# Optimization experiments

Measured on AMD Instinct MI355X. Metric: run time of the kernel, lower is better.

Reference implementation:

```python
import jax, jax.numpy as jnp
import numpy as np

B, T, V, LMAX = 32, 1024, 1024, 128
BLANK = 0
NEG = jnp.float32(-1e30)


def setup_inputs() -> dict:
    key = jax.random.key(0)
    k1, k2, k3, k4 = jax.random.split(key, 4)
    ys_hat = jax.random.normal(k1, (B, T, V), dtype=jnp.float32)
    ys_pad = jax.random.randint(k2, (B, LMAX), 1, V, dtype=jnp.int32)  # no blanks in labels
    hlens = jax.random.randint(k3, (B,), T // 2, T + 1, dtype=jnp.int32)
    ys_lens = jax.random.randint(k4, (B,), LMAX // 2, LMAX + 1, dtype=jnp.int32)
    return {"ys_hat": ys_hat, "ys_pad": ys_pad, "hlens": hlens, "ys_lens": ys_lens}


def _ctc_neg_log_lik(log_probs, ys_pad, hlens, ys_lens):
    # log_probs: [B, T, V] log-softmaxed frame activations
    b, t, v = log_probs.shape
    lmax = ys_pad.shape[1]
    s = 2 * lmax + 1  # extended label length (blanks interleaved)
    # extended labels: blank, y1, blank, y2, ..., blank
    ext = jnp.full((b, s), BLANK, dtype=ys_pad.dtype).at[:, 1::2].set(ys_pad)  # [B, S]
    # gather per-frame log-probs of extended labels -> [B, T, S]
    lp_ext = jnp.take_along_axis(log_probs, jnp.broadcast_to(ext[:, None, :], (b, t, s)), axis=2)
    # skip transition allowed at s if ext[s] != blank and ext[s] != ext[s-2]
    ext_m2 = jnp.pad(ext[:, :-2], ((0, 0), (2, 0)), constant_values=BLANK)
    skip = (jnp.arange(s)[None, :] >= 2) & (ext != BLANK) & (ext != ext_m2)  # [B, S]

    def shift(a, n):
        return jnp.pad(a[:, :-n], ((0, 0), (n, 0)), constant_values=NEG)

    # t = 0: paths can start at s=0 (blank) or s=1 (first label)
    alpha0 = jnp.full((b, s), NEG, dtype=log_probs.dtype)
    alpha0 = alpha0.at[:, 0].set(lp_ext[:, 0, 0]).at[:, 1].set(lp_ext[:, 0, 1])

    def step(alpha, inp):
        tt, lp_t = inp  # lp_t: [B, S]
        cand = jnp.logaddexp(alpha, shift(alpha, 1))
        cand = jnp.logaddexp(cand, jnp.where(skip, shift(alpha, 2), NEG))
        new = cand + lp_t
        alpha = jnp.where((tt < hlens)[:, None], new, alpha)  # freeze past each hlen
        return alpha, None

    ts = jnp.arange(1, t)
    alpha, _ = jax.lax.scan(step, alpha0, (ts, jnp.swapaxes(lp_ext, 0, 1)[1:]))

    # terminal states: s = 2*ys_len (final blank) or 2*ys_len - 1 (last label)
    i1 = (2 * ys_lens)[:, None]
    i2 = (2 * ys_lens - 1)[:, None]
    a1 = jnp.take_along_axis(alpha, i1, axis=1)[:, 0]
    a2 = jnp.take_along_axis(alpha, i2, axis=1)[:, 0]
    return -jnp.logaddexp(a1, a2)  # [B]


def reference(ys_hat, ys_pad, hlens, ys_lens):
    # log_softmax over vocab, then CTC forward DP; reduction='sum' then / B
    log_probs = jax.nn.log_softmax(ys_hat, axis=-1)
    losses = _ctc_neg_log_lik(log_probs, ys_pad, hlens, ys_lens)
    return jnp.sum(losses) / ys_hat.shape[0]
```

## Files before the change

kernel.cpp:

```cpp
#include <hip/hip_runtime.h>
#include <math.h>

#define BB    32
#define TT    1024
#define VV    1024
#define LM    128
#define SS    257
#define SP    272
#define RNORM 16
#define PF    16
#define RPW   8

__global__ __launch_bounds__(256) void ctc_row_kernel(
    const float* __restrict__ ys_hat, const int* __restrict__ ys_pad,
    const int* __restrict__ hlens, float* __restrict__ lp,
    float* __restrict__ out)
{
    __shared__ float srow[4][VV];
    if (blockIdx.x == 0 && threadIdx.x == 0) *out = 0.f;
    const int w    = threadIdx.x >> 6;
    const int lane = threadIdx.x & 63;
    const int gw   = blockIdx.x * 4 + w;
    const int b    = gw >> 7;
    const int t0   = (gw & 127) * RPW;
    const int hl   = hlens[b];
    int nrows = hl - t0;
    if (nrows <= 0) return;
    if (nrows > RPW) nrows = RPW;

    const int lab0 = ys_pad[b * LM + 2 * lane];
    const int lab1 = ys_pad[b * LM + 2 * lane + 1];
    const float* xr  = ys_hat + ((size_t)b * TT + t0) * VV;
    float*       lpo = lp     + ((size_t)b * TT + t0) * SP;

    float4 va0, va1, va2, va3, vb0, vb1, vb2, vb3;
    {
        const float4* cx = (const float4*)xr;
        va0 = cx[lane]; va1 = cx[lane + 64]; va2 = cx[lane + 128]; va3 = cx[lane + 192];
    }

#define ROW_STEP(C0, C1, C2, C3, N0, N1, N2, N3)                               \
    {                                                                          \
        if (i + 1 < nrows) {   \
            const float4* nx = (const float4*)(xr + (size_t)(i + 1) * VV);     \
            N0 = nx[lane]; N1 = nx[lane + 64];                                 \
            N2 = nx[lane + 128]; N3 = nx[lane + 192];                          \
        }                                                                      \
        float4* sw = (float4*)srow[w];                                         \
        sw[lane] = C0; sw[lane + 64] = C1;                                     \
        sw[lane + 128] = C2; sw[lane + 192] = C3;                              \
        float m = fmaxf(fmaxf(fmaxf(C0.x, C0.y), fmaxf(C0.z, C0.w)),          \
                        fmaxf(fmaxf(C1.x, C1.y), fmaxf(C1.z, C1.w)));          \
        m = fmaxf(m, fmaxf(fmaxf(fmaxf(C2.x, C2.y), fmaxf(C2.z, C2.w)),       \
                           fmaxf(fmaxf(C3.x, C3.y), fmaxf(C3.z, C3.w))));      \
        float s = __expf(C0.x - m) + __expf(C0.y - m) + __expf(C0.z - m) +     \
                  __expf(C0.w - m) + __expf(C1.x - m) + __expf(C1.y - m) +     \
                  __expf(C1.z - m) + __expf(C1.w - m) + __expf(C2.x - m) +     \
                  __expf(C2.y - m) + __expf(C2.z - m) + __expf(C2.w - m) +     \
                  __expf(C3.x - m) + __expf(C3.y - m) + __expf(C3.z - m) +     \
                  __expf(C3.w - m);                                            \
        _Pragma("unroll")                                                      \
        for (int off = 32; off; off >>= 1) {      \
            const float mo = __shfl_xor(m, off);                               \
            const float so = __shfl_xor(s, off);                               \
            const float mn = fmaxf(m, mo);                                     \
            s = s * __expf(m - mn) + so * __expf(mo - mn);                     \
            m = mn;                                                            \
        }                                                                      \
        const float xbv = srow[w][0];                                          \
        const float x1v = srow[w][lab0];                                       \
        const float x3v = srow[w][lab1];                                       \
        ((float2*)(lpo + (size_t)i * SP))[lane] =                              \
            make_float2(__expf(x1v - xbv), __expf(x3v - xbv));                 \
        if (lane < 16) {               \
            float val = 0.f;                                                   \
            if (lane == 0) val = __logf(s) + (m - xbv);     \
            lpo[(size_t)i * SP + 256 + lane] = val;                            \
        }                                                                      \
    }

    int i = 0;
    for (;;) {
        ROW_STEP(va0, va1, va2, va3, vb0, vb1, vb2, vb3)
        if (++i >= nrows) break;
        ROW_STEP(vb0, vb1, vb2, vb3, va0, va1, va2, va3)
        if (++i >= nrows) break;
    }
#undef ROW_STEP
}

#define DPP_ADDF(x, ctrl)                                                       \
    x = x + __int_as_float(__builtin_amdgcn_update_dpp(                         \
            0, __float_as_int(x), ctrl, 0xf, 0xf, true))
#define DPP_IMAX(x, ctrl)                                                       \
    {                                                                           \
        const int _o = __builtin_amdgcn_update_dpp(0, x, ctrl, 0xf, 0xf, true); \
        x = (x > _o) ? x : _o;                                                  \
    }
#define RLANEF(x, l) __int_as_float(__builtin_amdgcn_readlane(__float_as_int(x), (l)))
#define RLANEI(x, l) __builtin_amdgcn_readlane((x), (l))

__device__ __forceinline__ double dpp_wave_shr1_f64(double x)
{
    const int lo = __builtin_amdgcn_update_dpp(
        0, __double2loint(x), 0x138, 0xf, 0xf, true);
    const int hi = __builtin_amdgcn_update_dpp(
        0, __double2hiint(x), 0x138, 0xf, 0xf, true);
    return __hiloint2double(hi, lo);
}

__global__ __launch_bounds__(64, 1) void ctc_dp_kernel(
    const float* __restrict__ lp_all, const int* __restrict__ ys_pad,
    const int* __restrict__ hlens, const int* __restrict__ ys_lens,
    float* __restrict__ out)
{
    __shared__ double sh[SS];
    const int b    = blockIdx.x;
    const int lane = threadIdx.x;
    const int hl   = hlens[b];
    const float* lp = lp_all + (size_t)b * TT * SP;

    float sv[16];
#pragma unroll
    for (int jj = 0; jj < 16; ++jj)
        sv[jj] = lp[(size_t)(lane + jj * 64) * SP + 256];

    float2 qr[PF];
#pragma unroll
    for (int j = 0; j < PF; ++j)
        qr[j] = ((const float2*)(lp + (size_t)(1 + j) * SP))[lane];

    const int* lab = ys_pad + b * LM;
    const double sk1d = (lane > 0 && lab[2 * lane] != lab[2 * lane - 1]) ? 1.0 : 0.0;
    const double sk3d = (lab[2 * lane + 1] != lab[2 * lane]) ? 1.0 : 0.0;

    float ssv = 0.f;
#pragma unroll
    for (int jj = 0; jj < 16; ++jj)
        ssv += (lane + jj * 64 < hl) ? sv[jj] : 0.f;
    DPP_ADDF(ssv, 0x111); DPP_ADDF(ssv, 0x112); DPP_ADDF(ssv, 0x114); DPP_ADDF(ssv, 0x118);
    const float ssw = RLANEF(ssv, 15) + RLANEF(ssv, 31) + RLANEF(ssv, 47) + RLANEF(ssv, 63);

    const float2 q0 = ((const float2*)lp)[lane];
    double a0 = (lane == 0) ? 1.0 : 0.0;
    double a1 = (lane == 0) ? (double)q0.x : 0.0;
    double a2 = 0.0, a3 = 0.0, a4 = 0.0;
    int ksum = 0;

#define RENORM_BODY                                                            \
    {                                                                          \
        double m = fmax(fmax(fmax(a0, a1), fmax(a2, a3)), a4);                 \
        m = fmax(m, 1e-300);                          \
        int hi = __double2hiint(m);            \
        DPP_IMAX(hi, 0x111); DPP_IMAX(hi, 0x112);                              \
        DPP_IMAX(hi, 0x114); DPP_IMAX(hi, 0x118);                              \
        const int h0 = RLANEI(hi, 15), h1 = RLANEI(hi, 31);                    \
        const int h2 = RLANEI(hi, 47), h3 = RLANEI(hi, 63);                    \
        int hw = (h0 > h1) ? h0 : h1;                                          \
        hw = (hw > h2) ? hw : h2;                                              \
        hw = (hw > h3) ? hw : h3;                                              \
        const int k = (hw >> 20) - 1022;             \
        const double sc = __hiloint2double((1023 - k) << 20, 0);  \
        ksum += k;                           \
        a0 *= sc; a1 *= sc; a2 *= sc; a3 *= sc; a4 *= sc;                      \
    }

#define DP_STEP(q)                                                             \
    {                                                                          \
        const double ry = (double)(q).x;            \
        const double rw = (double)(q).y;            \
        const double n1 = dpp_wave_shr1_f64(a3);   \
        const double c0 = a0 + n1;                          \
        const double c1 = fma(sk1d, n1, a0 + a1) * ry;                         \
        const double c2 = a2 + a1;                          \
        const double c3 = (a3 + fma(sk3d, a1, a2)) * rw;                       \
        const double c4 = a4 + a3;              \
        a0 = c0; a1 = c1; a2 = c2; a3 = c3; a4 = c4;                           \
    }

    int t0 = 1;
    for (; t0 + 2 * PF - 1 <= hl - 1; t0 += PF) {
        const float* pfp = lp + (size_t)(t0 + PF) * SP;
#pragma unroll
        for (int j = 0; j < PF; ++j) {
            const float2 q = qr[j];
            qr[j] = ((const float2*)(pfp + (size_t)j * SP))[lane];
            if (j == PF - 1) RENORM_BODY
            DP_STEP(q)
        }
    }
    for (; t0 < hl; t0 += PF) {
#pragma unroll
        for (int j = 0; j < PF; ++j) {
            const int t = t0 + j;
            const float2 q = qr[j];
            int tp = t + PF; if (tp > hl - 1) tp = hl - 1;
            qr[j] = ((const float2*)(lp + (size_t)tp * SP))[lane];
            if (t < hl) {
                if ((t & (RNORM - 1)) == 0) RENORM_BODY
                DP_STEP(q)
            }
        }
    }
#undef DP_STEP
#undef RENORM_BODY

    sh[4 * lane]     = a0;
    sh[4 * lane + 1] = a1;
    sh[4 * lane + 2] = a2;
    sh[4 * lane + 3] = a3;
    if (lane == 63) sh[256] = a4;
    __syncthreads();
    if (lane == 0) {
        const int L = ys_lens[b];
        const double aL = sh[2 * L] + sh[2 * L - 1];
        const double loss = (double)ssw -
            (log(aL) + (double)ksum * 0.6931471805599453);
        atomicAdd(out, (float)(loss * (1.0 / (double)BB)));
    }
}

extern "C" void kernel_launch(void* const* d_in, const int* in_sizes, int n_in,
                              void* d_out, int out_size, void* d_ws, size_t ws_size,
                              hipStream_t stream) {
    const float* ys_hat  = (const float*)d_in[0];
    const int*   ys_pad  = (const int*)d_in[1];
    const int*   hlens   = (const int*)d_in[2];
    const int*   ys_lens = (const int*)d_in[3];
    float* out = (float*)d_out;

    float* lp_raw = (float*)d_ws;

    ctc_row_kernel<<<BB * TT / (4 * RPW), 256, 0, stream>>>(ys_hat, ys_pad, hlens, lp_raw, out);
    ctc_dp_kernel<<<BB, 64, 0, stream>>>(lp_raw, ys_pad, hlens, ys_lens, out);
}
```

Baseline: 251.8 us.

## Switch CTC alpha recursion to fp32 with per-lane exponent scaling

Moves the serial DP recursion from double to float and replaces the wave-wide max renormalisation with a per-lane exponent. Each lane keeps its own scale, and values passed in by DPP are rescaled by the exponent difference between neighbouring lanes. Renormalisation now runs every 4 steps, with no cross-lane reduction, so it stays local. This removes fp64 arithmetic and the cross-lane reduce and readlane operations from the latency-critical chain. In exchange, each step does extra integer work for the neighbour scale, and float underflow could hurt accuracy.

```diff
diff --git a/kernel.cpp b/kernel.cpp
--- a/kernel.cpp
+++ b/kernel.cpp
@@ -7,7 +7,7 @@
 #define LM    128
 #define SS    257
 #define SP    272
-#define RNORM 16
+#define RNORM 4
 #define PF    16
 #define RPW   8
 
@@ -92,21 +92,16 @@
 #define DPP_ADDF(x, ctrl)                                                       \
     x = x + __int_as_float(__builtin_amdgcn_update_dpp(                         \
             0, __float_as_int(x), ctrl, 0xf, 0xf, true))
-#define DPP_IMAX(x, ctrl)                                                       \
-    {                                                                           \
-        const int _o = __builtin_amdgcn_update_dpp(0, x, ctrl, 0xf, 0xf, true); \
-        x = (x > _o) ? x : _o;                                                  \
-    }
 #define RLANEF(x, l) __int_as_float(__builtin_amdgcn_readlane(__float_as_int(x), (l)))
-#define RLANEI(x, l) __builtin_amdgcn_readlane((x), (l))
-
-__device__ __forceinline__ double dpp_wave_shr1_f64(double x)
-{
-    const int lo = __builtin_amdgcn_update_dpp(
-        0, __double2loint(x), 0x138, 0xf, 0xf, true);
-    const int hi = __builtin_amdgcn_update_dpp(
-        0, __double2hiint(x), 0x138, 0xf, 0xf, true);
-    return __hiloint2double(hi, lo);
+
+__device__ __forceinline__ float dpp_shr1_f32(float x)
+{
+    return __int_as_float(__builtin_amdgcn_update_dpp(
+        0, __float_as_int(x), 0x138, 0xf, 0xf, true));
+}
+__device__ __forceinline__ int dpp_shr1_i32(int x)
+{
+    return __builtin_amdgcn_update_dpp(0, x, 0x138, 0xf, 0xf, true);
 }
 
 __global__ __launch_bounds__(64, 1) void ctc_dp_kernel(
@@ -114,7 +109,8 @@
     const int* __restrict__ hlens, const int* __restrict__ ys_lens,
     float* __restrict__ out)
 {
-    __shared__ double sh[SS];
+    __shared__ float sh[SS];
+    __shared__ int   shk[64];
     const int b    = blockIdx.x;
     const int lane = threadIdx.x;
     const int hl   = hlens[b];
@@ -131,8 +127,8 @@
         qr[j] = ((const float2*)(lp + (size_t)(1 + j) * SP))[lane];
 
     const int* lab = ys_pad + b * LM;
-    const double sk1d = (lane > 0 && lab[2 * lane] != lab[2 * lane - 1]) ? 1.0 : 0.0;
-    const double sk3d = (lab[2 * lane + 1] != lab[2 * lane]) ? 1.0 : 0.0;
+    const float sk1f = (lane > 0 && lab[2 * lane] != lab[2 * lane - 1]) ? 1.0f : 0.0f;
+    const float sk3f = (lab[2 * lane + 1] != lab[2 * lane]) ? 1.0f : 0.0f;
 
     float ssv = 0.f;
 #pragma unroll
@@ -142,39 +138,40 @@
     const float ssw = RLANEF(ssv, 15) + RLANEF(ssv, 31) + RLANEF(ssv, 47) + RLANEF(ssv, 63);
 
     const float2 q0 = ((const float2*)lp)[lane];
-    double a0 = (lane == 0) ? 1.0 : 0.0;
-    double a1 = (lane == 0) ? (double)q0.x : 0.0;
-    double a2 = 0.0, a3 = 0.0, a4 = 0.0;
-    int ksum = 0;
+    float a0 = (lane == 0) ? 1.0f : 0.0f;
+    float a1 = (lane == 0) ? q0.x : 0.0f;
+    float a2 = 0.0f, a3 = 0.0f, a4 = 0.0f;
+    int   kl = 0;
+    bool  live = (lane == 0);
 
 #define RENORM_BODY                                                            \
     {                                                                          \
-        double m = fmax(fmax(fmax(a0, a1), fmax(a2, a3)), a4);                 \
-        m = fmax(m, 1e-300);                          \
-        int hi = __double2hiint(m);            \
-        DPP_IMAX(hi, 0x111); DPP_IMAX(hi, 0x112);                              \
-        DPP_IMAX(hi, 0x114); DPP_IMAX(hi, 0x118);                              \
-        const int h0 = RLANEI(hi, 15), h1 = RLANEI(hi, 31);                    \
-        const int h2 = RLANEI(hi, 47), h3 = RLANEI(hi, 63);                    \
-        int hw = (h0 > h1) ? h0 : h1;                                          \
-        hw = (hw > h2) ? hw : h2;                                              \
-        hw = (hw > h3) ? hw : h3;                                              \
-        const int k = (hw >> 20) - 1022;             \
-        const double sc = __hiloint2double((1023 - k) << 20, 0);  \
-        ksum += k;                           \
+        float m = fmaxf(fmaxf(fmaxf(a0, a1), fmaxf(a2, a3)), a4);              \
+        const int e = (__float_as_int(m) >> 23) - 126;     \
+        const float sc = __int_as_float((127 - e) << 23);      \
+        kl += e;                         \
         a0 *= sc; a1 *= sc; a2 *= sc; a3 *= sc; a4 *= sc;                      \
     }
 
 #define DP_STEP(q)                                                             \
     {                                                                          \
-        const double ry = (double)(q).x;            \
-        const double rw = (double)(q).y;            \
-        const double n1 = dpp_wave_shr1_f64(a3);   \
-        const double c0 = a0 + n1;                          \
-        const double c1 = fma(sk1d, n1, a0 + a1) * ry;                         \
-        const double c2 = a2 + a1;                          \
-        const double c3 = (a3 + fma(sk3d, a1, a2)) * rw;                       \
-        const double c4 = a4 + a3;              \
+        const float ry = (q).x;                     \
+        const float rw = (q).y;                     \
+        const float n1r = dpp_shr1_f32(a3);           \
+        const int   kp  = dpp_shr1_i32(kl);                 \
+        int d = kp - kl;                                                       \
+        d = d < -127 ? -127 : (d > 127 ? 127 : d);                             \
+        float ds = __int_as_float((127 + d) << 23);    \
+        const bool wk = (!live) && (n1r > 0.0f);        \
+        kl = wk ? kp : kl;                                                     \
+        ds = wk ? 1.0f : ds;                                                   \
+        live = live || wk;                                                     \
+        const float n1 = n1r * ds;                    \
+        const float c0 = a0 + n1;                           \
+        const float c1 = fmaf(sk1f, n1, a0 + a1) * ry;                         \
+        const float c2 = a2 + a1;                           \
+        const float c3 = (a3 + fmaf(sk3f, a1, a2)) * rw;                       \
+        const float c4 = a4 + a3;               \
         a0 = c0; a1 = c1; a2 = c2; a3 = c3; a4 = c4;                           \
     }
 
@@ -185,8 +182,8 @@
         for (int j = 0; j < PF; ++j) {
             const float2 q = qr[j];
             qr[j] = ((const float2*)(pfp + (size_t)j * SP))[lane];
-            if (j == PF - 1) RENORM_BODY
             DP_STEP(q)
+            if ((j & 3) == 3) RENORM_BODY
         }
     }
     for (; t0 < hl; t0 += PF) {
@@ -197,8 +194,8 @@
             int tp = t + PF; if (tp > hl - 1) tp = hl - 1;
             qr[j] = ((const float2*)(lp + (size_t)tp * SP))[lane];
             if (t < hl) {
+                DP_STEP(q)
                 if ((t & (RNORM - 1)) == 0) RENORM_BODY
-                DP_STEP(q)
             }
         }
     }
@@ -209,13 +206,22 @@
     sh[4 * lane + 1] = a1;
     sh[4 * lane + 2] = a2;
     sh[4 * lane + 3] = a3;
+    shk[lane]        = kl;
     if (lane == 63) sh[256] = a4;
     __syncthreads();
     if (lane == 0) {
-        const int L = ys_lens[b];
-        const double aL = sh[2 * L] + sh[2 * L - 1];
+        const int L  = ys_lens[b];
+        const int s1 = 2 * L, s2 = 2 * L - 1;
+        const float v1 = sh[s1], v2 = sh[s2];
+        const int l1 = (s1 >> 2) > 63 ? 63 : (s1 >> 2);
+        const int k1 = shk[l1], k2 = shk[s2 >> 2];
+        const int km = (k1 > k2) ? k1 : k2;
+        int d1 = 127 + (k1 - km); if (d1 < 0) d1 = 0;
+        int d2 = 127 + (k2 - km); if (d2 < 0) d2 = 0;
+        const double w1 = (double)v1 * (double)__int_as_float(d1 << 23);
+        const double w2 = (double)v2 * (double)__int_as_float(d2 << 23);
         const double loss = (double)ssw -
-            (log(aL) + (double)ksum * 0.6931471805599453);
+            (log(w1 + w2) + (double)km * 0.6931471805599453);
         atomicAdd(out, (float)(loss * (1.0 / (double)BB)));
     }
 }
```

Measured after the change: 265.7 us. 1.06x slower.

## Split CTC DP into concurrent forward and backward waves meeting at midpoint

Applied to the files above, without the earlier changes.

The CTC recursion kernel now runs two waves per batch item. One computes the forward alpha recursion up to hl/2 and the other computes a backward beta recursion from hl-1 down to hl/2. The two are combined through shared memory with a transition-weighted dot product. This roughly halves the serial dependency chain of the latency-bound DP. In exchange it adds backward-step logic, a second renormalisation sum, and an extra cross-wave merge.

```diff
diff --git a/kernel.cpp b/kernel.cpp
--- a/kernel.cpp
+++ b/kernel.cpp
@@ -108,44 +108,38 @@
         0, __double2hiint(x), 0x138, 0xf, 0xf, true);
     return __hiloint2double(hi, lo);
 }
-
-__global__ __launch_bounds__(64, 1) void ctc_dp_kernel(
+__device__ __forceinline__ double dpp_wave_shl1_f64(double x)
+{
+    const int lo = __builtin_amdgcn_update_dpp(
+        0, __double2loint(x), 0x130, 0xf, 0xf, true);
+    const int hi = __builtin_amdgcn_update_dpp(
+        0, __double2hiint(x), 0x130, 0xf, 0xf, true);
+    return __hiloint2double(hi, lo);
+}
+
+__global__ __launch_bounds__(128, 1) void ctc_dp_kernel(
     const float* __restrict__ lp_all, const int* __restrict__ ys_pad,
     const int* __restrict__ hlens, const int* __restrict__ ys_lens,
     float* __restrict__ out)
 {
-    __shared__ double sh[SS];
+    __shared__ double shb[SS + 1];
+    __shared__ int    shk[2];
+    const int wid  = threadIdx.x >> 6;
+    const int lane = threadIdx.x & 63;
     const int b    = blockIdx.x;
-    const int lane = threadIdx.x;
     const int hl   = hlens[b];
+    const int mid  = hl >> 1;
     const float* lp = lp_all + (size_t)b * TT * SP;
-
-    float sv[16];
-#pragma unroll
-    for (int jj = 0; jj < 16; ++jj)
-        sv[jj] = lp[(size_t)(lane + jj * 64) * SP + 256];
-
-    float2 qr[PF];
-#pragma unroll
-    for (int j = 0; j < PF; ++j)
-        qr[j] = ((const float2*)(lp + (size_t)(1 + j) * SP))[lane];
-
-    const int* lab = ys_pad + b * LM;
+    const int*  lab = ys_pad + b * LM;
+
     const double sk1d = (lane > 0 && lab[2 * lane] != lab[2 * lane - 1]) ? 1.0 : 0.0;
     const double sk3d = (lab[2 * lane + 1] != lab[2 * lane]) ? 1.0 : 0.0;
-
-    float ssv = 0.f;
-#pragma unroll
-    for (int jj = 0; jj < 16; ++jj)
-        ssv += (lane + jj * 64 < hl) ? sv[jj] : 0.f;
-    DPP_ADDF(ssv, 0x111); DPP_ADDF(ssv, 0x112); DPP_ADDF(ssv, 0x114); DPP_ADDF(ssv, 0x118);
-    const float ssw = RLANEF(ssv, 15) + RLANEF(ssv, 31) + RLANEF(ssv, 47) + RLANEF(ssv, 63);
-
-    const float2 q0 = ((const float2*)lp)[lane];
-    double a0 = (lane == 0) ? 1.0 : 0.0;
-    double a1 = (lane == 0) ? (double)q0.x : 0.0;
-    double a2 = 0.0, a3 = 0.0, a4 = 0.0;
+    const double skBd = (lane < 63 && lab[2 * lane + 2] != lab[2 * lane + 1]) ? 1.0 : 0.0;
+
+    double a0 = 0.0, a1 = 0.0, a2 = 0.0, a3 = 0.0, a4 = 0.0;
     int ksum = 0;
+    float ssw = 0.f;
+    float2 qr[PF];
 
 #define RENORM_BODY                                                            \
     {                                                                          \
@@ -160,63 +154,151 @@
         hw = (hw > h2) ? hw : h2;                                              \
         hw = (hw > h3) ? hw : h3;                                              \
         const int k = (hw >> 20) - 1022;             \
-        const double sc = __hiloint2double((1023 - k) << 20, 0);  \
-        ksum += k;                           \
+        const double sc = __hiloint2double((1023 - k) << 20, 0);     \
+        ksum += k;                                                             \
         a0 *= sc; a1 *= sc; a2 *= sc; a3 *= sc; a4 *= sc;                      \
     }
 
-#define DP_STEP(q)                                                             \
+#define FWD_STEP(q)                                                            \
     {                                                                          \
-        const double ry = (double)(q).x;            \
-        const double rw = (double)(q).y;            \
-        const double n1 = dpp_wave_shr1_f64(a3);   \
-        const double c0 = a0 + n1;                          \
+        const double ry = (double)(q).x;                                       \
+        const double rw = (double)(q).y;                                       \
+        const double n1 = dpp_wave_shr1_f64(a3);      \
+        const double c0 = a0 + n1;                                             \
         const double c1 = fma(sk1d, n1, a0 + a1) * ry;                         \
-        const double c2 = a2 + a1;                          \
+        const double c2 = a2 + a1;                                             \
         const double c3 = (a3 + fma(sk3d, a1, a2)) * rw;                       \
-        const double c4 = a4 + a3;              \
+        const double c4 = a4 + a3;           \
         a0 = c0; a1 = c1; a2 = c2; a3 = c3; a4 = c4;                           \
     }
 
-    int t0 = 1;
-    for (; t0 + 2 * PF - 1 <= hl - 1; t0 += PF) {
-        const float* pfp = lp + (size_t)(t0 + PF) * SP;
-#pragma unroll
-        for (int j = 0; j < PF; ++j) {
-            const float2 q = qr[j];
-            qr[j] = ((const float2*)(pfp + (size_t)j * SP))[lane];
-            if (j == PF - 1) RENORM_BODY
-            DP_STEP(q)
-        }
-    }
-    for (; t0 < hl; t0 += PF) {
-#pragma unroll
-        for (int j = 0; j < PF; ++j) {
-            const int t = t0 + j;
-            const float2 q = qr[j];
-            int tp = t + PF; if (tp > hl - 1) tp = hl - 1;
-            qr[j] = ((const float2*)(lp + (size_t)tp * SP))[lane];
-            if (t < hl) {
-                if ((t & (RNORM - 1)) == 0) RENORM_BODY
-                DP_STEP(q)
+#define BWD_STEP(q)                                                            \
+    {                                                                          \
+        const double r0  = (double)(q).x;          \
+        const double r1  = (double)(q).y;          \
+        const double n0  = dpp_wave_shl1_f64(a0);   \
+        const double n1b = dpp_wave_shl1_f64(a1);   \
+        const double x   = (lane == 63) ? a4 : n0;        \
+        const double c0 = a0 + a1;                     \
+        const double c1 = fma(sk3d, a3, a1 + a2) * r0;                         \
+        const double c2 = a2 + a3;                                             \
+        const double c3 = (a3 + fma(skBd, n1b, x)) * r1;                       \
+        a0 = c0; a1 = c1; a2 = c2; a3 = c3;      \
+    }
+
+    if (wid == 0) {
+        float sv[16];
+#pragma unroll
+        for (int jj = 0; jj < 16; ++jj)
+            sv[jj] = lp[(size_t)(lane + jj * 64) * SP + 256];
+#pragma unroll
+        for (int j = 0; j < PF; ++j)
+            qr[j] = ((const float2*)(lp + (size_t)(1 + j) * SP))[lane];
+        float ssv = 0.f;
+#pragma unroll
+        for (int jj = 0; jj < 16; ++jj)
+            ssv += (lane + jj * 64 < hl) ? sv[jj] : 0.f;
+        DPP_ADDF(ssv, 0x111); DPP_ADDF(ssv, 0x112);
+        DPP_ADDF(ssv, 0x114); DPP_ADDF(ssv, 0x118);
+        ssw = RLANEF(ssv, 15) + RLANEF(ssv, 31) + RLANEF(ssv, 47) + RLANEF(ssv, 63);
+
+        const float2 q0 = ((const float2*)lp)[lane];
+        a0 = (lane == 0) ? 1.0 : 0.0;
+        a1 = (lane == 0) ? (double)q0.x : 0.0;
+
+        int t0 = 1;
+        for (; t0 + 2 * PF - 1 <= mid - 1; t0 += PF) {
+            const float* pfp = lp + (size_t)(t0 + PF) * SP;
+#pragma unroll
+            for (int j = 0; j < PF; ++j) {
+                const float2 q = qr[j];
+                qr[j] = ((const float2*)(pfp + (size_t)j * SP))[lane];
+                if (j == PF - 1) RENORM_BODY
+                FWD_STEP(q)
             }
         }
-    }
-#undef DP_STEP
+        for (; t0 < mid; t0 += PF) {
+#pragma unroll
+            for (int j = 0; j < PF; ++j) {
+                const int t = t0 + j;
+                const float2 q = qr[j];
+                int tp = t + PF; if (tp > hl - 1) tp = hl - 1;
+                qr[j] = ((const float2*)(lp + (size_t)tp * SP))[lane];
+                if (t < mid) {
+                    if ((t & (RNORM - 1)) == 0) RENORM_BODY
+                    FWD_STEP(q)
+                }
+            }
+        }
+    } else {
+        const int L  = ys_lens[b];
+        const int sA = 2 * L;
+        const int sB = 2 * L - 1;
+        const float2 qe = ((const float2*)(lp + (size_t)(hl - 1) * SP))[lane];
+        a0 = (4 * lane     == sA) ? 1.0 : 0.0;
+        a2 = (4 * lane + 2 == sA) ? 1.0 : 0.0;
+        a1 = (4 * lane + 1 == sB) ? (double)qe.x : 0.0;
+        a3 = (4 * lane + 3 == sB) ? (double)qe.y : 0.0;
+        a4 = (sA == 256 && lane == 63) ? 1.0 : 0.0;
+
+#pragma unroll
+        for (int j = 0; j < PF; ++j)
+            qr[j] = ((const float2*)(lp + (size_t)(hl - 2 - j) * SP))[lane];
+
+        int tt = hl - 2;
+        for (; tt - (2 * PF - 1) >= mid; tt -= PF) {
+#pragma unroll
+            for (int j = 0; j < PF; ++j) {
+                const float2 q = qr[j];
+                qr[j] = ((const float2*)(lp + (size_t)(tt - PF - j) * SP))[lane];
+                if (j == PF - 1) RENORM_BODY
+                BWD_STEP(q)
+            }
+        }
+        for (; tt >= mid; tt -= PF) {
+#pragma unroll
+            for (int j = 0; j < PF; ++j) {
+                const int t = tt - j;
+                const float2 q = qr[j];
+                int tq = tt - PF - j; if (tq < 0) tq = 0;
+                qr[j] = ((const float2*)(lp + (size_t)tq * SP))[lane];
+                if (t >= mid) {
+                    if ((t & (RNORM - 1)) == 0) RENORM_BODY
+                    BWD_STEP(q)
+                }
+            }
+        }
+        shb[4 * lane]     = a0;
+        shb[4 * lane + 1] = a1;
+        shb[4 * lane + 2] = a2;
+        shb[4 * lane + 3] = a3;
+        if (lane == 63) { shb[256] = a4; shb[257] = 0.0; }
+    }
+#undef FWD_STEP
+#undef BWD_STEP
 #undef RENORM_BODY
 
-    sh[4 * lane]     = a0;
-    sh[4 * lane + 1] = a1;
-    sh[4 * lane + 2] = a2;
-    sh[4 * lane + 3] = a3;
-    if (lane == 63) sh[256] = a4;
+    if (lane == 0) shk[wid] = ksum;
     __syncthreads();
-    if (lane == 0) {
-        const int L = ys_lens[b];
-        const double aL = sh[2 * L] + sh[2 * L - 1];
-        const double loss = (double)ssw -
-            (log(aL) + (double)ksum * 0.6931471805599453);
-        atomicAdd(out, (float)(loss * (1.0 / (double)BB)));
+
+    if (wid == 0) {
+        const double b0  = shb[4 * lane],     b1  = shb[4 * lane + 1];
+        const double b2  = shb[4 * lane + 2], b3  = shb[4 * lane + 3];
+        const double b4r = shb[4 * lane + 4];
+        const double b5r = shb[4 * lane + 5];
+        const double g0 = b0 + b1;
+        const double g1 = fma(sk3d, b3, b1 + b2);
+        const double g2 = b2 + b3;
+        const double g3 = fma(skBd, b5r, b3 + b4r);
+        double c = a0 * g0 + a1 * g1 + a2 * g2 + a3 * g3;
+        if (lane == 63) c += a4 * shb[256];
+#pragma unroll
+        for (int off = 32; off; off >>= 1) c += __shfl_xor(c, off);
+        if (lane == 0) {
+            const double loss = (double)ssw -
+                (log(c) + (double)(shk[0] + shk[1]) * 0.6931471805599453);
+            atomicAdd(out, (float)(loss * (1.0 / (double)BB)));
+        }
     }
 }
 
@@ -232,5 +314,5 @@
     float* lp_raw = (float*)d_ws;
 
     ctc_row_kernel<<<BB * TT / (4 * RPW), 256, 0, stream>>>(ys_hat, ys_pad, hlens, lp_raw, out);
-    ctc_dp_kernel<<<BB, 64, 0, stream>>>(lp_raw, ys_pad, hlens, ys_lens, out);
-}
+    ctc_dp_kernel<<<BB, 128, 0, stream>>>(lp_raw, ys_pad, hlens, ys_lens, out);
+}
```

Result: faster. 228.4 us (-9.3%).
